# Performance work log

Measured on AMD Instinct MI355X. Metric: run time of the kernel, lower is better.

The kernel has to match this reference:

```python
import jax, jax.numpy as jnp
import numpy as np

V = 32000   # input_size == output_size (vocab)
E = 512     # embedding_dim
H = 1024    # hidden_dim
B = 32      # batch
S = 64      # source length
T = 64      # target length
SOS = 1     # Vocabulary.special_tokens['<sos>']


def setup_inputs() -> dict:
    key = jax.random.key(0)
    ks = jax.random.split(key, 24)
    sc_e = 1.0 / np.sqrt(H)
    d = {
        'input_seq': jax.random.randint(ks[0], (B, S), 0, V),
        'target_seq': jax.random.randint(ks[1], (B, T), 0, V),
        'emb': jax.random.normal(ks[2], (V, E), jnp.float32) * 0.02,
        'fc_W': jax.random.normal(ks[3], (V, H), jnp.float32) * sc_e,
        'fc_b': jnp.zeros((V,), jnp.float32),
    }
    i = 4
    for pre in ('enc', 'dec'):
        for l, in_dim in ((0, E), (1, H)):
            d[f'{pre}_Wih{l}'] = jax.random.normal(ks[i], (4 * H, in_dim), jnp.float32) * sc_e; i += 1
            d[f'{pre}_Whh{l}'] = jax.random.normal(ks[i], (4 * H, H), jnp.float32) * sc_e; i += 1
            d[f'{pre}_bih{l}'] = jnp.zeros((4 * H,), jnp.float32)
            d[f'{pre}_bhh{l}'] = jnp.zeros((4 * H,), jnp.float32)
    return d


def _lstm_cell(x, h, c, Wih, Whh, bih, bhh):
    # PyTorch gate order: i, f, g, o
    g = x @ Wih.T + h @ Whh.T + (bih + bhh)
    i, f, gg, o = jnp.split(g, 4, axis=-1)
    c = jax.nn.sigmoid(f) * c + jax.nn.sigmoid(i) * jnp.tanh(gg)
    h = jax.nn.sigmoid(o) * jnp.tanh(c)
    return h, c


def _run_lstm(x_tbe, h0, c0, h1, c1, Wih0, Whh0, bih0, bhh0, Wih1, Whh1, bih1, bhh1):
    # x_tbe: [T, B, in]; 2-layer LSTM, returns top-layer hiddens [T, B, H] and final state
    def step(carry, x_t):
        h0, c0, h1, c1 = carry
        h0, c0 = _lstm_cell(x_t, h0, c0, Wih0, Whh0, bih0, bhh0)
        h1, c1 = _lstm_cell(h0, h1, c1, Wih1, Whh1, bih1, bhh1)
        return (h0, c0, h1, c1), h1
    carry, hs = jax.lax.scan(step, (h0, c0, h1, c1), x_tbe)
    return carry, hs


def reference(input_seq, target_seq, emb, fc_W, fc_b,
              enc_Wih0, enc_Whh0, enc_bih0, enc_bhh0,
              enc_Wih1, enc_Whh1, enc_bih1, enc_bhh1,
              dec_Wih0, dec_Whh0, dec_bih0, dec_bhh0,
              dec_Wih1, dec_Whh1, dec_bih1, dec_bhh1):
    b = input_seq.shape[0]
    z = jnp.zeros((b, H), emb.dtype)
    # --- encoder over source sequence ---
    enc_in = emb[input_seq].transpose(1, 0, 2)  # [S, B, E]
    (h0, c0, h1, c1), _ = _run_lstm(enc_in, z, z, z, z,
                                    enc_Wih0, enc_Whh0, enc_bih0, enc_bhh0,
                                    enc_Wih1, enc_Whh1, enc_bih1, enc_bhh1)
    # --- decoder: full teacher forcing -> inputs are [<sos>, target[:, :-1]] ---
    dec_ids = jnp.concatenate([jnp.full((b, 1), SOS, target_seq.dtype),
                               target_seq[:, :-1]], axis=1)
    dec_in = emb[dec_ids].transpose(1, 0, 2)  # [T, B, E]
    _, dec_hs = _run_lstm(dec_in, h0, c0, h1, c1,
                          dec_Wih0, dec_Whh0, dec_bih0, dec_bhh0,
                          dec_Wih1, dec_Whh1, dec_bih1, dec_bhh1)
    # fc applied per step (linear, so one batched matmul is identical math)
    logits = jnp.einsum('tbh,vh->btv', dec_hs, fc_W) + fc_b  # [B, T, V]
    return logits
```

## Files before the change

### kernel.cpp

```cpp
#include <hip/hip_runtime.h>

#define DEVINL __device__ __forceinline__

typedef unsigned short u16;
typedef __attribute__((ext_vector_type(8))) short v8s;
typedef __attribute__((ext_vector_type(4))) short v4s;
typedef __attribute__((ext_vector_type(4))) float v4f;

static constexpr int Vn = 32000, En = 512, Hn = 1024, Bn = 32, Tn = 64;
static constexpr int FH = 4096;
static constexpr int MR = 2048;
static constexpr int BH = Bn * Hn;

DEVINL u16 f2bf(float x) {
    unsigned u = __float_as_uint(x);
    return (u16)((u + 0x7FFFu + ((u >> 16) & 1u)) >> 16);
}
DEVINL float bf2f(u16 h) { return __uint_as_float(((unsigned)h) << 16); }
DEVINL void split2(float x, u16 &hi, u16 &lo) {
    u16 h = f2bf(x);
    hi = h;
    lo = f2bf(x - bf2f(h));
}
DEVINL float sigm(float x) { return 1.f / (1.f + __expf(-x)); }
DEVINL float tanh_fast(float x) { return 1.f - 2.f / (__expf(2.f * x) + 1.f); }
DEVINL v4f mf(v8s a, v8s b, v4f c) { return __builtin_amdgcn_mfma_f32_16x16x32_bf16(a, b, c, 0, 0, 0); }
DEVINL v8s cat8(v4s a, v4s b) { return __builtin_shufflevector(a, b, 0, 1, 2, 3, 4, 5, 6, 7); }

DEVINL void gload_lds16(const u16* g, u16* l) {
    __builtin_amdgcn_global_load_lds((const __attribute__((address_space(1))) void*)g,
                                     (__attribute__((address_space(3))) void*)l, 16, 0, 0);
}

static constexpr int BAR_U32 = 16 + 256 * 16 + 256 * 16;
__global__ void bar_init(unsigned* bar) {
    for (int i = threadIdx.x; i < BAR_U32; i += 256) bar[i] = 0u;
}

__global__ void gather_split(const float* __restrict__ emb, const int* __restrict__ seq,
                             int isdec, u16* __restrict__ xh, u16* __restrict__ xl) {
    const int m = blockIdx.x;
    const int b = m & 31, t = m >> 5;
    const int id = isdec ? (t == 0 ? 1 : seq[b * 64 + t - 1]) : seq[b * 64 + t];
    const float* src = emb + (size_t)id * En;
    for (int e = threadIdx.x; e < En; e += 256) {
        u16 h, l; split2(src[e], h, l);
        xh[(size_t)m * En + e] = h;
        xl[(size_t)m * En + e] = l;
    }
}

__global__ void split_w(const float* __restrict__ W, u16* __restrict__ hi,
                        u16* __restrict__ lo, int n4) {
    const int stride = gridDim.x * blockDim.x;
    for (int i = blockIdx.x * blockDim.x + threadIdx.x; i < n4; i += stride) {
        float4 x = ((const float4*)W)[i];
        u16 h0,h1,h2,h3,l0,l1,l2,l3;
        split2(x.x,h0,l0); split2(x.y,h1,l1); split2(x.z,h2,l2); split2(x.w,h3,l3);
        ushort4 hv; hv.x=h0; hv.y=h1; hv.z=h2; hv.w=h3;
        ((ushort4*)hi)[i] = hv;
        if (lo) { ushort4 lv; lv.x=l0; lv.y=l1; lv.z=l2; lv.w=l3; ((ushort4*)lo)[i] = lv; }
    }
}

__global__ void perm_split(const float* __restrict__ Whh, u16* __restrict__ ph,
                           u16* __restrict__ pl) {
    const int g = blockIdx.x;
    const int q = g >> 10, j = g & 1023;
    const int dst = (j >> 2) * 16 + q * 4 + (j & 3);
    const int k4 = threadIdx.x;
    float4 x = ((const float4*)(Whh + (size_t)g * Hn))[k4];
    u16 h0,h1,h2,h3,l0,l1,l2,l3;
    split2(x.x,h0,l0); split2(x.y,h1,l1); split2(x.z,h2,l2); split2(x.w,h3,l3);
    ushort4 hv; hv.x=h0; hv.y=h1; hv.z=h2; hv.w=h3;
    ushort4 lv; lv.x=l0; lv.y=l1; lv.z=l2; lv.w=l3;
    ((ushort4*)(ph + (size_t)dst * Hn))[k4] = hv;
    ((ushort4*)(pl + (size_t)dst * Hn))[k4] = lv;
}

__global__ void unperm_h(const u16* __restrict__ ph, const u16* __restrict__ pl,
                         u16* __restrict__ oh, u16* __restrict__ ol) {
    const int m = blockIdx.x, t = m >> 5, b = m & 31;
    const int e = threadIdx.x;
    const size_t src = (size_t)t * BH + (size_t)e * 128 + b * 4;
    const size_t dst = (size_t)m * Hn + (size_t)e * 4;
    *(v4s*)(oh + dst) = *(const v4s*)(ph + src);
    *(v4s*)(ol + dst) = *(const v4s*)(pl + src);
}

template<int TERMS, int MODE>
__global__ __launch_bounds__(256)
void gemm_bt(const u16* __restrict__ Ahi, const u16* __restrict__ Alo,
             const u16* __restrict__ Bhi, const u16* __restrict__ Blo,
             const float* __restrict__ bias1, const float* __restrict__ bias2,
             float* __restrict__ Cout, int M, int N, int K) {
    constexpr bool AL = (TERMS >= 2), BL = (TERMS >= 3);
    __shared__ __align__(16) u16 sAh[128 * 32];
    __shared__ __align__(16) u16 sBh[128 * 32];
    __shared__ __align__(16) u16 sAl[AL ? 128 * 32 : 8];
    __shared__ __align__(16) u16 sBl[BL ? 128 * 32 : 8];

    const int tid = threadIdx.x;
    const int lane = tid & 63, wave = tid >> 6;
    const int wr = wave >> 1, wc = wave & 1;
    const int nwgx = gridDim.x;
    const int nwg = nwgx * gridDim.y;
    int wg = blockIdx.y * nwgx + blockIdx.x;
    wg = (wg & 7) * (nwg >> 3) + (wg >> 3);
    const int m0 = (wg / nwgx) * 128, n0 = (wg % nwgx) * 128;
    const int fr = lane & 15, fk = lane >> 4;

    v4f acc[4][4];
#pragma unroll
    for (int i = 0; i < 4; ++i)
#pragma unroll
        for (int j = 0; j < 4; ++j) acc[i][j] = (v4f){0.f, 0.f, 0.f, 0.f};

    const int c0 = tid, c1 = tid + 256;
    const int r0 = c0 >> 2, kg0 = c0 & 3, r1 = c1 >> 2, kg1 = c1 & 3;
    const int cw0 = (tid & ~63) * 8;
    const int cw1 = cw0 + 256 * 8;

    for (int kk = 0; kk < K; kk += 32) {
        const size_t a0 = (size_t)(m0 + r0) * K + kk + kg0 * 8;
        const size_t a1 = (size_t)(m0 + r1) * K + kk + kg1 * 8;
        const size_t b0 = (size_t)(n0 + r0) * K + kk + kg0 * 8;
        const size_t b1 = (size_t)(n0 + r1) * K + kk + kg1 * 8;
        gload_lds16(Ahi + a0, sAh + cw0);
        gload_lds16(Ahi + a1, sAh + cw1);
        gload_lds16(Bhi + b0, sBh + cw0);
        gload_lds16(Bhi + b1, sBh + cw1);
        if constexpr (AL) {
            gload_lds16(Alo + a0, sAl + cw0);
            gload_lds16(Alo + a1, sAl + cw1);
        }
        if constexpr (BL) {
            gload_lds16(Blo + b0, sBl + cw0);
            gload_lds16(Blo + b1, sBl + cw1);
        }
        __syncthreads();

        v8s ah[4], bh[4], al[4], bl[4];
#pragma unroll
        for (int mt = 0; mt < 4; ++mt) {
            const int row = wr * 64 + mt * 16 + fr;
            const int idx = row * 32 + fk * 8;
            ah[mt] = *(const v8s*)(sAh + idx);
            if constexpr (AL) al[mt] = *(const v8s*)(sAl + idx);
        }
#pragma unroll
        for (int nt = 0; nt < 4; ++nt) {
            const int row = wc * 64 + nt * 16 + fr;
            const int idx = row * 32 + fk * 8;
            bh[nt] = *(const v8s*)(sBh + idx);
            if constexpr (BL) bl[nt] = *(const v8s*)(sBl + idx);
        }
#pragma unroll
        for (int mt = 0; mt < 4; ++mt)
#pragma unroll
            for (int nt = 0; nt < 4; ++nt) {
                acc[mt][nt] = mf(ah[mt], bh[nt], acc[mt][nt]);
                if constexpr (AL) acc[mt][nt] = mf(al[mt], bh[nt], acc[mt][nt]);
                if constexpr (BL) acc[mt][nt] = mf(ah[mt], bl[nt], acc[mt][nt]);
            }
        __syncthreads();
    }

#pragma unroll
    for (int nt = 0; nt < 4; ++nt) {
        const int col = n0 + wc * 64 + nt * 16 + fr;
        float bsum = bias1 ? bias1[col] : 0.f;
        if (bias2) bsum += bias2[col];
#pragma unroll
        for (int mt = 0; mt < 4; ++mt) {
            const int rowb = m0 + wr * 64 + mt * 16 + fk * 4;
#pragma unroll
            for (int p = 0; p < 4; ++p) {
                const int row = rowb + p;
                const float v = acc[mt][nt][p] + bsum;
                if constexpr (MODE == 2) {
                    const int t = row >> 5, b = row & 31;
                    Cout[(size_t)b * ((size_t)Tn * Vn) + (size_t)t * Vn + col] = v;
                } else if constexpr (MODE == 1) {
                    const int q = col >> 10, j = col & 1023;
                    const int bidw = j >> 2, rloc = (j & 3) * 4 + q;
                    Cout[(size_t)bidw * ((size_t)MR * 16) + (size_t)row * 16 + rloc] = v;
                } else {
                    Cout[(size_t)row * N + col] = v;
                }
            }
        }
    }
}

DEVINL void wait_flags(unsigned* flags, unsigned tgt) {
    if (threadIdx.x < 256) {
        while (__hip_atomic_load(&flags[threadIdx.x * 16], __ATOMIC_RELAXED, __HIP_MEMORY_SCOPE_AGENT) < tgt)
            __builtin_amdgcn_s_sleep(1);
    }
    __syncthreads();
}
DEVINL void signal_phase(unsigned* flags, unsigned val) {
    __syncthreads();
    if (threadIdx.x == 0)
        __hip_atomic_store(&flags[blockIdx.x * 16], val, __ATOMIC_RELAXED, __HIP_MEMORY_SCOPE_AGENT);
}

#define DECLW(P) v8s P##0, P##1, P##2, P##3
#define LOADW(P, BASE) do { const u16* _b = (BASE) + woff; \
    P##0 = *(const v8s*)(_b);       P##1 = *(const v8s*)(_b + 32); \
    P##2 = *(const v8s*)(_b + 64);  P##3 = *(const v8s*)(_b + 96); } while (0)
#define PINW(P) asm volatile("" : "+v"(P##0), "+v"(P##1), "+v"(P##2), "+v"(P##3))

#define LD8(B, B0, RO) cat8(*(const v4s*)((B) + (size_t)(B0) * 128 + (RO)), \
                            *(const v4s*)((B) + (size_t)(B0) * 128 + 128 + (RO)))

#define KT0(K) { \
    const int b0 = wave * 32 + K * 8 + fk * 2; \
    v8s hah = LD8(h0sh, b0, fr4); \
    v8s hal = LD8(h0sl, b0, fr4); \
    v8s hbh = LD8(h0sh, b0, fr4 + 64); \
    v8s hbl = LD8(h0sl, b0, fr4 + 64); \
    if (doL0) { \
        r0a = mf(hah, w0h_##K, r0a); r0a = mf(hal, w0h_##K, r0a); r0a = mf(hah, w0l_##K, r0a); \
        r0b = mf(hbh, w0h_##K, r0b); r0b = mf(hbl, w0h_##K, r0b); r0b = mf(hbh, w0l_##K, r0b); } \
    if (doL1) { \
        r1a = mf(hah, wih_##K, r1a); r1a = mf(hal, wih_##K, r1a); r1a = mf(hah, wil_##K, r1a); \
        r1b = mf(hbh, wih_##K, r1b); r1b = mf(hbl, wih_##K, r1b); r1b = mf(hbh, wil_##K, r1b); } }

#define KT1(K) { \
    const int b0 = wave * 32 + K * 8 + fk * 2; \
    v8s hah = LD8(h1sh, b0, fr4); \
    v8s hal = LD8(h1sl, b0, fr4); \
    v8s hbh = LD8(h1sh, b0, fr4 + 64); \
    v8s hbl = LD8(h1sl, b0, fr4 + 64); \
    r1a = mf(hah, w1h_##K, r1a); r1a = mf(hal, w1h_##K, r1a); r1a = mf(hah, w1l_##K, r1a); \
    r1b = mf(hbh, w1h_##K, r1b); r1b = mf(hbl, w1h_##K, r1b); r1b = mf(hbh, w1l_##K, r1b); }

__global__ __launch_bounds__(512, 2)
void lstm_scan2(const u16* __restrict__ W0h, const u16* __restrict__ W0l,
                const u16* __restrict__ WIh, const u16* __restrict__ WIl,
                const u16* __restrict__ W1h, const u16* __restrict__ W1l,
                const float* __restrict__ G0,
                const float* __restrict__ bi1, const float* __restrict__ bh1,
                const u16* __restrict__ s0h, const u16* __restrict__ s0l,
                const u16* __restrict__ s1h, const u16* __restrict__ s1l,
                u16* __restrict__ h0ha, u16* __restrict__ h0la,
                u16* __restrict__ h1ha, u16* __restrict__ h1la,
                u16* __restrict__ hs_h, u16* __restrict__ hs_l,
                const float* __restrict__ c0i, const float* __restrict__ c1i,
                float* __restrict__ c0o, float* __restrict__ c1o,
                unsigned* bar, int pbase, int initfs) {
    __shared__ float red0[8][32][17];
    __shared__ float red1[8][32][17];
    const int tid = threadIdx.x, lane = tid & 63, wave = tid >> 6, bid = blockIdx.x;
    const int fr = lane & 15, fk = lane >> 4;
    const int fr4 = fr * 4;
    const size_t woff = (size_t)(bid * 16 + fr) * Hn + wave * 128 + fk * 8;
    unsigned* flagsA = bar + 16;
    unsigned* flagsB = bar + 16 + 256 * 16;

    DECLW(w0h_); DECLW(w0l_); DECLW(wih_); DECLW(wil_); DECLW(w1h_); DECLW(w1l_);
    LOADW(w0h_, W0h); LOADW(w0l_, W0l);
    LOADW(wih_, WIh); LOADW(wil_, WIl);
    LOADW(w1h_, W1h); LOADW(w1l_, W1l);
    PINW(w0h_); PINW(w0l_); PINW(wih_); PINW(wil_); PINW(w1h_); PINW(w1l_);

    const int lt = tid & 127, cb = lt >> 2, cu = lt & 3, cj = bid * 4 + cu;
    const bool isL0 = tid < 128;
    const bool isL1 = (tid >= 128) && (tid < 256);
    float creg = 0.f;
    float b1v[4];
    if (isL0) {
        if (initfs) creg = c0i[cb * Hn + cj];
    } else if (isL1) {
        if (initfs) creg = c1i[cb * Hn + cj];
#pragma unroll
        for (int q = 0; q < 4; ++q) b1v[q] = bi1[q * Hn + cj] + bh1[q * Hn + cj];
    }

    for (int p = 0; p <= 64; ++p) {
        const bool doL0 = (p < 64), doL1 = (p >= 1);
        const bool hasH0 = (p > 0) || (initfs != 0);
        const bool hasH1 = doL1 && ((p > 1) || (initfs != 0));
        const u16* h0sh = (p == 0) ? s0h : h0ha + (size_t)(p - 1) * BH;
        const u16* h0sl = (p == 0) ? s0l : h0la + (size_t)(p - 1) * BH;
        const u16* h1sh = (p <= 1) ? s1h : h1ha + (size_t)(p - 2) * BH;
        const u16* h1sl = (p <= 1) ? s1l : h1la + (size_t)(p - 2) * BH;

        v4f gq = (v4f){0.f, 0.f, 0.f, 0.f};
        if (isL0 && doL0)
            gq = *(const v4f*)(G0 + (size_t)bid * ((size_t)MR * 16)
                               + (size_t)(p * 32 + cb) * 16 + cu * 4);

        if (p >= 1) wait_flags(flagsA, (unsigned)(pbase + p));

        v4f r0a = {0,0,0,0}, r0b = {0,0,0,0}, r1a = {0,0,0,0}, r1b = {0,0,0,0};
        if (hasH0) {
            KT0(0) KT0(1) KT0(2) KT0(3)
        }
        if (doL0 && hasH0) {
#pragma unroll
            for (int pp = 0; pp < 4; ++pp) {
                red0[wave][fk * 4 + pp][fr]      = r0a[pp];
                red0[wave][fk * 4 + pp + 16][fr] = r0b[pp];
            }
        }
        __syncthreads();

        if (isL0 && doL0) {
            float gv[4];
#pragma unroll
            for (int q = 0; q < 4; ++q) {
                const int rr = q * 4 + cu;
                float s = 0.f;
                if (hasH0) {
#pragma unroll
                    for (int wv = 0; wv < 8; ++wv) s += red0[wv][cb][rr];
                }
                gv[q] = s + gq[q];
            }
            const float gi = sigm(gv[0]), gf = sigm(gv[1]);
            const float gg = tanh_fast(gv[2]), go = sigm(gv[3]);
            creg = gf * creg + gi * gg;
            const float h = go * tanh_fast(creg);
            u16 hh, hl; split2(h, hh, hl);
            const unsigned prh = (unsigned)(u16)__shfl_xor((int)hh, 1);
            const unsigned prl = (unsigned)(u16)__shfl_xor((int)hl, 1);
            if ((cu & 1) == 0) {
                const size_t ho2 = (size_t)p * (BH / 2) + bid * 64 + cb * 2 + (cu >> 1);
                __hip_atomic_store((unsigned*)h0ha + ho2, (prh << 16) | hh,
                                   __ATOMIC_RELAXED, __HIP_MEMORY_SCOPE_AGENT);
                __hip_atomic_store((unsigned*)h0la + ho2, (prl << 16) | hl,
                                   __ATOMIC_RELAXED, __HIP_MEMORY_SCOPE_AGENT);
            }
            if (p == 63) {
                c0o[cb * Hn + cj] = creg;
                if (hs_h) {
                    hs_h[bid * 128 + cb * 4 + cu] = hh;
                    hs_l[bid * 128 + cb * 4 + cu] = hl;
                }
            }
        }
        signal_phase(flagsA, (unsigned)(pbase + p + 1));

        if (p >= 2) wait_flags(flagsB, (unsigned)(pbase + p));

        if (hasH1) {
            KT1(0) KT1(1) KT1(2) KT1(3)
        }
        if (doL1) {
#pragma unroll
            for (int pp = 0; pp < 4; ++pp) {
                red1[wave][fk * 4 + pp][fr]      = r1a[pp];
                red1[wave][fk * 4 + pp + 16][fr] = r1b[pp];
            }
        }
        __syncthreads();

        if (isL1 && doL1) {
            const int t1 = p - 1;
            float gv[4];
#pragma unroll
            for (int q = 0; q < 4; ++q) {
                const int rr = q * 4 + cu;
                float s = b1v[q];
#pragma unroll
                for (int wv = 0; wv < 8; ++wv) s += red1[wv][cb][rr];
                gv[q] = s;
            }
            const float gi = sigm(gv[0]), gf = sigm(gv[1]);
            const float gg = tanh_fast(gv[2]), go = sigm(gv[3]);
            creg = gf * creg + gi * gg;
            const float h = go * tanh_fast(creg);
            u16 hh, hl; split2(h, hh, hl);
            const unsigned prh = (unsigned)(u16)__shfl_xor((int)hh, 1);
            const unsigned prl = (unsigned)(u16)__shfl_xor((int)hl, 1);
            if ((cu & 1) == 0) {
                const size_t ho2 = (size_t)t1 * (BH / 2) + bid * 64 + cb * 2 + (cu >> 1);
                __hip_atomic_store((unsigned*)h1ha + ho2, (prh << 16) | hh,
                                   __ATOMIC_RELAXED, __HIP_MEMORY_SCOPE_AGENT);
                __hip_atomic_store((unsigned*)h1la + ho2, (prl << 16) | hl,
                                   __ATOMIC_RELAXED, __HIP_MEMORY_SCOPE_AGENT);
            }
            if (t1 == 63) c1o[cb * Hn + cj] = creg;
        }
        signal_phase(flagsB, (unsigned)(pbase + p + 1));
    }
}

extern "C" void kernel_launch(void* const* d_in, const int* in_sizes, int n_in,
                              void* d_out, int out_size, void* d_ws, size_t ws_size,
                              hipStream_t stream) {
    (void)in_sizes; (void)n_in; (void)out_size; (void)ws_size;
    const int*   input_seq  = (const int*)d_in[0];
    const int*   target_seq = (const int*)d_in[1];
    const float* emb  = (const float*)d_in[2];
    const float* fc_W = (const float*)d_in[3];
    const float* fc_b = (const float*)d_in[4];
    const float* W_ih[4] = {(const float*)d_in[5],  (const float*)d_in[9],
                            (const float*)d_in[13], (const float*)d_in[17]};
    const float* W_hh[4] = {(const float*)d_in[6],  (const float*)d_in[10],
                            (const float*)d_in[14], (const float*)d_in[18]};
    const float* b_ih[4] = {(const float*)d_in[7],  (const float*)d_in[11],
                            (const float*)d_in[15], (const float*)d_in[19]};
    const float* b_hh[4] = {(const float*)d_in[8],  (const float*)d_in[12],
                            (const float*)d_in[16], (const float*)d_in[20]};

    char* w = (char*)d_ws;
    size_t off = 0;
    auto alloc = [&](size_t bytes) {
        void* p = (void*)(w + off);
        off += (bytes + 255) & ~(size_t)255;
        return p;
    };
    unsigned* bar = (unsigned*)alloc(BAR_U32 * 4);
    float* G   = (float*)alloc((size_t)MR * FH * 4);
    u16* W0h   = (u16*)alloc((size_t)FH * Hn * 2);
    u16* W0l   = (u16*)alloc((size_t)FH * Hn * 2);
    u16* WIh   = (u16*)alloc((size_t)FH * Hn * 2);
    u16* WIl   = (u16*)alloc((size_t)FH * Hn * 2);
    u16* W1h   = (u16*)alloc((size_t)FH * Hn * 2);
    u16* W1l   = (u16*)alloc((size_t)FH * Hn * 2);
    u16* SWh   = (u16*)alloc((size_t)FH * Hn * 2);
    u16* SWl   = (u16*)alloc((size_t)FH * Hn * 2);
    u16* Xh    = (u16*)alloc((size_t)MR * En * 2);
    u16* Xl    = (u16*)alloc((size_t)MR * En * 2);
    u16* hAh   = (u16*)alloc((size_t)Tn * BH * 2);
    u16* hAl   = (u16*)alloc((size_t)Tn * BH * 2);
    u16* hBh   = (u16*)alloc((size_t)Tn * BH * 2);
    u16* hBl   = (u16*)alloc((size_t)Tn * BH * 2);
    u16* hs0h  = (u16*)alloc((size_t)BH * 2);
    u16* hs0l  = (u16*)alloc((size_t)BH * 2);
    float* c0  = (float*)alloc((size_t)BH * 4);
    float* c1  = (float*)alloc((size_t)BH * 4);
    u16* hFh   = (u16*)alloc((size_t)MR * Hn * 2);
    u16* hFl   = (u16*)alloc((size_t)MR * Hn * 2);
    u16* fWh = (u16*)G;

    bar_init<<<1, 256, 0, stream>>>(bar);

    auto scan = [&](const u16* s0hp, const u16* s0lp, const u16* s1hp, const u16* s1lp,
                    u16* hsh, u16* hsl, const float* bi1, const float* bh1,
                    int pbase, int fs) {
        const u16 *a0=W0h,*a1=W0l,*a2=WIh,*a3=WIl,*a4=W1h,*a5=W1l;
        const float* Gp = G;
        u16 *p0=hAh,*p1=hAl,*p2=hBh,*p3=hBl;
        const float *ci0=c0,*ci1=c1; float *co0=c0,*co1=c1;
        unsigned* bp = bar;
        void* args[] = {(void*)&a0,(void*)&a1,(void*)&a2,(void*)&a3,(void*)&a4,(void*)&a5,
                        (void*)&Gp,(void*)&bi1,(void*)&bh1,
                        (void*)&s0hp,(void*)&s0lp,(void*)&s1hp,(void*)&s1lp,
                        (void*)&p0,(void*)&p1,(void*)&p2,(void*)&p3,
                        (void*)&hsh,(void*)&hsl,
                        (void*)&ci0,(void*)&ci1,(void*)&co0,(void*)&co1,
                        (void*)&bp,(void*)&pbase,(void*)&fs};
        if (hipLaunchCooperativeKernel((void*)lstm_scan2, dim3(256), dim3(512),
                                       args, 0, stream) != hipSuccess) {
            lstm_scan2<<<dim3(256), dim3(512), 0, stream>>>(
                W0h, W0l, WIh, WIl, W1h, W1l, G, bi1, bh1,
                s0hp, s0lp, s1hp, s1lp, hAh, hAl, hBh, hBl, hsh, hsl,
                c0, c1, c0, c1, bar, pbase, fs);
        }
    };

    const size_t lastT = (size_t)63 * BH;

    gather_split<<<MR, 256, 0, stream>>>(emb, input_seq, 0, Xh, Xl);
    split_w<<<2048, 256, 0, stream>>>(W_ih[0], SWh, SWl, FH * En / 4);
    gemm_bt<3, 1><<<dim3(FH / 128, MR / 128), 256, 0, stream>>>(
        Xh, Xl, SWh, SWl, b_ih[0], b_hh[0], G, MR, FH, En);
    perm_split<<<FH, 256, 0, stream>>>(W_hh[0], W0h, W0l);
    perm_split<<<FH, 256, 0, stream>>>(W_ih[1], WIh, WIl);
    perm_split<<<FH, 256, 0, stream>>>(W_hh[1], W1h, W1l);
    scan(hs0h, hs0l, hs0h, hs0l, hs0h, hs0l, b_ih[1], b_hh[1], 0, 0);

    gather_split<<<MR, 256, 0, stream>>>(emb, target_seq, 1, Xh, Xl);
    split_w<<<2048, 256, 0, stream>>>(W_ih[2], SWh, SWl, FH * En / 4);
    gemm_bt<3, 1><<<dim3(FH / 128, MR / 128), 256, 0, stream>>>(
        Xh, Xl, SWh, SWl, b_ih[2], b_hh[2], G, MR, FH, En);
    perm_split<<<FH, 256, 0, stream>>>(W_hh[2], W0h, W0l);
    perm_split<<<FH, 256, 0, stream>>>(W_ih[3], WIh, WIl);
    perm_split<<<FH, 256, 0, stream>>>(W_hh[3], W1h, W1l);
    scan(hs0h, hs0l, hBh + lastT, hBl + lastT, nullptr, nullptr,
         b_ih[3], b_hh[3], 130, 1);

    unperm_h<<<MR, 256, 0, stream>>>(hBh, hBl, hFh, hFl);
    split_w<<<2048, 256, 0, stream>>>(fc_W, fWh, nullptr, Vn * Hn / 4);
    gemm_bt<2, 2><<<dim3(Vn / 128, MR / 128), 256, 0, stream>>>(
        hFh, hFl, fWh, nullptr, fc_b, nullptr, (float*)d_out, MR, Vn, Hn);
}
```

Measured before the change: 1.431 ms.

## Split LSTM scan block into layer-0 and layer-1 wave groups with LDS barriers

The persistent LSTM scan kernel previously ran both layers in lockstep across all 8 waves, using block-wide __syncthreads and grid flag waits. Now waves 0-3 handle layer 0 alone, with its recurrent weights held in registers, and waves 4-7 handle layer 1. The layer-1 waves stream their input and recurrent weights from global memory each step. The two groups sync through LDS atomic counters instead of __syncthreads, so layer 0 of step t+1 can overlap layer 1 of step t. The trade is reloading layer-1 weights from memory every step, plus spin-wait overhead and more reliance on careful memory ordering.

New measurement: 2.185 ms. 1.53x slower.

```diff
diff --git a/kernel.cpp b/kernel.cpp
--- a/kernel.cpp
+++ b/kernel.cpp
@@ -193,49 +193,64 @@
     }
 }
 
-DEVINL void wait_flags(unsigned* flags, unsigned tgt) {
-    if (threadIdx.x < 256) {
-        while (__hip_atomic_load(&flags[threadIdx.x * 16], __ATOMIC_RELAXED, __HIP_MEMORY_SCOPE_AGENT) < tgt)
+DEVINL void poll4(unsigned* flags, unsigned tgt, int lane) {
+#pragma unroll
+    for (int j = 0; j < 4; ++j) {
+        unsigned* p = flags + (size_t)(lane + j * 64) * 16;
+        while (__hip_atomic_load(p, __ATOMIC_RELAXED, __HIP_MEMORY_SCOPE_AGENT) < tgt)
             __builtin_amdgcn_s_sleep(1);
     }
-    __syncthreads();
-}
-DEVINL void signal_phase(unsigned* flags, unsigned val) {
-    __syncthreads();
-    if (threadIdx.x == 0)
-        __hip_atomic_store(&flags[blockIdx.x * 16], val, __ATOMIC_RELAXED, __HIP_MEMORY_SCOPE_AGENT);
-}
-
-#define DECLW(P) v8s P##0, P##1, P##2, P##3
-#define LOADW(P, BASE) do { const u16* _b = (BASE) + woff; \
+}
+DEVINL void lds_arrive(unsigned* c) {
+    __hip_atomic_fetch_add(c, 1u, __ATOMIC_RELEASE, __HIP_MEMORY_SCOPE_WORKGROUP);
+}
+DEVINL void lds_spin(unsigned* c, unsigned tgt) {
+    while (__hip_atomic_load(c, __ATOMIC_ACQUIRE, __HIP_MEMORY_SCOPE_WORKGROUP) < tgt)
+        __builtin_amdgcn_s_sleep(0);
+}
+
+#define DECLW8(P) v8s P##0, P##1, P##2, P##3, P##4, P##5, P##6, P##7
+#define LOADW8(P, BASE) do { const u16* _b = (BASE) + woff; \
     P##0 = *(const v8s*)(_b);       P##1 = *(const v8s*)(_b + 32); \
-    P##2 = *(const v8s*)(_b + 64);  P##3 = *(const v8s*)(_b + 96); } while (0)
-#define PINW(P) asm volatile("" : "+v"(P##0), "+v"(P##1), "+v"(P##2), "+v"(P##3))
+    P##2 = *(const v8s*)(_b + 64);  P##3 = *(const v8s*)(_b + 96); \
+    P##4 = *(const v8s*)(_b + 128); P##5 = *(const v8s*)(_b + 160); \
+    P##6 = *(const v8s*)(_b + 192); P##7 = *(const v8s*)(_b + 224); } while (0)
+#define PINW8(P) asm volatile("" : "+v"(P##0), "+v"(P##1), "+v"(P##2), "+v"(P##3), \
+                                   "+v"(P##4), "+v"(P##5), "+v"(P##6), "+v"(P##7))
 
 #define LD8(B, B0, RO) cat8(*(const v4s*)((B) + (size_t)(B0) * 128 + (RO)), \
                             *(const v4s*)((B) + (size_t)(B0) * 128 + 128 + (RO)))
 
-#define KT0(K) { \
-    const int b0 = wave * 32 + K * 8 + fk * 2; \
+#define KT0L(K) { \
+    const int b0 = wave * 64 + K * 8 + fk * 2; \
     v8s hah = LD8(h0sh, b0, fr4); \
     v8s hal = LD8(h0sl, b0, fr4); \
     v8s hbh = LD8(h0sh, b0, fr4 + 64); \
     v8s hbl = LD8(h0sl, b0, fr4 + 64); \
-    if (doL0) { \
-        r0a = mf(hah, w0h_##K, r0a); r0a = mf(hal, w0h_##K, r0a); r0a = mf(hah, w0l_##K, r0a); \
-        r0b = mf(hbh, w0h_##K, r0b); r0b = mf(hbl, w0h_##K, r0b); r0b = mf(hbh, w0l_##K, r0b); } \
-    if (doL1) { \
-        r1a = mf(hah, wih_##K, r1a); r1a = mf(hal, wih_##K, r1a); r1a = mf(hah, wil_##K, r1a); \
-        r1b = mf(hbh, wih_##K, r1b); r1b = mf(hbl, wih_##K, r1b); r1b = mf(hbh, wil_##K, r1b); } }
-
-#define KT1(K) { \
-    const int b0 = wave * 32 + K * 8 + fk * 2; \
+    r0a = mf(hah, w0h_##K, r0a); r0a = mf(hal, w0h_##K, r0a); r0a = mf(hah, w0l_##K, r0a); \
+    r0b = mf(hbh, w0h_##K, r0b); r0b = mf(hbl, w0h_##K, r0b); r0b = mf(hbh, w0l_##K, r0b); }
+
+#define KTIH(K) { \
+    const int b0 = w4 * 64 + K * 8 + fk * 2; \
+    v8s wih = *(const v8s*)(WIh + woffT + K * 32); \
+    v8s wil = *(const v8s*)(WIl + woffT + K * 32); \
+    v8s hah = LD8(h0sh, b0, fr4); \
+    v8s hal = LD8(h0sl, b0, fr4); \
+    v8s hbh = LD8(h0sh, b0, fr4 + 64); \
+    v8s hbl = LD8(h0sl, b0, fr4 + 64); \
+    r1a = mf(hah, wih, r1a); r1a = mf(hal, wih, r1a); r1a = mf(hah, wil, r1a); \
+    r1b = mf(hbh, wih, r1b); r1b = mf(hbl, wih, r1b); r1b = mf(hbh, wil, r1b); }
+
+#define KTH1(K) { \
+    const int b0 = w4 * 64 + K * 8 + fk * 2; \
+    v8s w1h = *(const v8s*)(W1h + woffT + K * 32); \
+    v8s w1l = *(const v8s*)(W1l + woffT + K * 32); \
     v8s hah = LD8(h1sh, b0, fr4); \
     v8s hal = LD8(h1sl, b0, fr4); \
     v8s hbh = LD8(h1sh, b0, fr4 + 64); \
     v8s hbl = LD8(h1sl, b0, fr4 + 64); \
-    r1a = mf(hah, w1h_##K, r1a); r1a = mf(hal, w1h_##K, r1a); r1a = mf(hah, w1l_##K, r1a); \
-    r1b = mf(hbh, w1h_##K, r1b); r1b = mf(hbl, w1h_##K, r1b); r1b = mf(hbh, w1l_##K, r1b); }
+    r1a = mf(hah, w1h, r1a); r1a = mf(hal, w1h, r1a); r1a = mf(hah, w1l, r1a); \
+    r1b = mf(hbh, w1h, r1b); r1b = mf(hbl, w1h, r1b); r1b = mf(hbh, w1l, r1b); }
 
 __global__ __launch_bounds__(512, 2)
 void lstm_scan2(const u16* __restrict__ W0h, const u16* __restrict__ W0l,
@@ -251,141 +266,151 @@
                 const float* __restrict__ c0i, const float* __restrict__ c1i,
                 float* __restrict__ c0o, float* __restrict__ c1o,
                 unsigned* bar, int pbase, int initfs) {
-    __shared__ float red0[8][32][17];
-    __shared__ float red1[8][32][17];
+    __shared__ float red0[4][32][17];
+    __shared__ float red1[4][32][17];
+    __shared__ unsigned cb4[4];
     const int tid = threadIdx.x, lane = tid & 63, wave = tid >> 6, bid = blockIdx.x;
     const int fr = lane & 15, fk = lane >> 4;
     const int fr4 = fr * 4;
-    const size_t woff = (size_t)(bid * 16 + fr) * Hn + wave * 128 + fk * 8;
     unsigned* flagsA = bar + 16;
     unsigned* flagsB = bar + 16 + 256 * 16;
-
-    DECLW(w0h_); DECLW(w0l_); DECLW(wih_); DECLW(wil_); DECLW(w1h_); DECLW(w1l_);
-    LOADW(w0h_, W0h); LOADW(w0l_, W0l);
-    LOADW(wih_, WIh); LOADW(wil_, WIl);
-    LOADW(w1h_, W1h); LOADW(w1l_, W1l);
-    PINW(w0h_); PINW(w0l_); PINW(wih_); PINW(wil_); PINW(w1h_); PINW(w1l_);
-
-    const int lt = tid & 127, cb = lt >> 2, cu = lt & 3, cj = bid * 4 + cu;
-    const bool isL0 = tid < 128;
-    const bool isL1 = (tid >= 128) && (tid < 256);
-    float creg = 0.f;
-    float b1v[4];
-    if (isL0) {
-        if (initfs) creg = c0i[cb * Hn + cj];
-    } else if (isL1) {
-        if (initfs) creg = c1i[cb * Hn + cj];
-#pragma unroll
-        for (int q = 0; q < 4; ++q) b1v[q] = bi1[q * Hn + cj] + bh1[q * Hn + cj];
-    }
-
-    for (int p = 0; p <= 64; ++p) {
-        const bool doL0 = (p < 64), doL1 = (p >= 1);
-        const bool hasH0 = (p > 0) || (initfs != 0);
-        const bool hasH1 = doL1 && ((p > 1) || (initfs != 0));
-        const u16* h0sh = (p == 0) ? s0h : h0ha + (size_t)(p - 1) * BH;
-        const u16* h0sl = (p == 0) ? s0l : h0la + (size_t)(p - 1) * BH;
-        const u16* h1sh = (p <= 1) ? s1h : h1ha + (size_t)(p - 2) * BH;
-        const u16* h1sl = (p <= 1) ? s1l : h1la + (size_t)(p - 2) * BH;
-
-        v4f gq = (v4f){0.f, 0.f, 0.f, 0.f};
-        if (isL0 && doL0)
-            gq = *(const v4f*)(G0 + (size_t)bid * ((size_t)MR * 16)
-                               + (size_t)(p * 32 + cb) * 16 + cu * 4);
-
-        if (p >= 1) wait_flags(flagsA, (unsigned)(pbase + p));
-
-        v4f r0a = {0,0,0,0}, r0b = {0,0,0,0}, r1a = {0,0,0,0}, r1b = {0,0,0,0};
-        if (hasH0) {
-            KT0(0) KT0(1) KT0(2) KT0(3)
-        }
-        if (doL0 && hasH0) {
+    if (tid == 0) { cb4[0] = 0; cb4[1] = 0; cb4[2] = 0; cb4[3] = 0; }
+    __syncthreads();
+
+    if (wave < 4) {
+        const size_t woff = (size_t)(bid * 16 + fr) * Hn + wave * 256 + fk * 8;
+        DECLW8(w0h_); DECLW8(w0l_);
+        LOADW8(w0h_, W0h); LOADW8(w0l_, W0l);
+        PINW8(w0h_); PINW8(w0l_);
+        const int lt = tid & 127, cbb = lt >> 2, cu = lt & 3, cj = bid * 4 + cu;
+        const bool isCell = tid < 128;
+        float creg = 0.f;
+        if (isCell && initfs) creg = c0i[cbb * Hn + cj];
+
+        for (int q = 0; q < 64; ++q) {
+            v4f gq = (v4f){0.f, 0.f, 0.f, 0.f};
+            if (isCell)
+                gq = *(const v4f*)(G0 + (size_t)bid * ((size_t)MR * 16)
+                                   + (size_t)(q * 32 + cbb) * 16 + cu * 4);
+            if (q >= 1) poll4(flagsA, (unsigned)(pbase + q), lane);
+            const bool hasH0 = (q > 0) || (initfs != 0);
+            const u16* h0sh = (q == 0) ? s0h : h0ha + (size_t)(q - 1) * BH;
+            const u16* h0sl = (q == 0) ? s0l : h0la + (size_t)(q - 1) * BH;
+            v4f r0a = {0,0,0,0}, r0b = {0,0,0,0};
+            if (hasH0) {
+                KT0L(0) KT0L(1) KT0L(2) KT0L(3) KT0L(4) KT0L(5) KT0L(6) KT0L(7)
+            }
 #pragma unroll
             for (int pp = 0; pp < 4; ++pp) {
                 red0[wave][fk * 4 + pp][fr]      = r0a[pp];
                 red0[wave][fk * 4 + pp + 16][fr] = r0b[pp];
             }
-        }
-        __syncthreads();
-
-        if (isL0 && doL0) {
-            float gv[4];
-#pragma unroll
-            for (int q = 0; q < 4; ++q) {
-                const int rr = q * 4 + cu;
-                float s = 0.f;
-                if (hasH0) {
-#pragma unroll
-                    for (int wv = 0; wv < 8; ++wv) s += red0[wv][cb][rr];
-                }
-                gv[q] = s + gq[q];
-            }
-            const float gi = sigm(gv[0]), gf = sigm(gv[1]);
-            const float gg = tanh_fast(gv[2]), go = sigm(gv[3]);
-            creg = gf * creg + gi * gg;
-            const float h = go * tanh_fast(creg);
-            u16 hh, hl; split2(h, hh, hl);
-            const unsigned prh = (unsigned)(u16)__shfl_xor((int)hh, 1);
-            const unsigned prl = (unsigned)(u16)__shfl_xor((int)hl, 1);
-            if ((cu & 1) == 0) {
-                const size_t ho2 = (size_t)p * (BH / 2) + bid * 64 + cb * 2 + (cu >> 1);
-                __hip_atomic_store((unsigned*)h0ha + ho2, (prh << 16) | hh,
-                                   __ATOMIC_RELAXED, __HIP_MEMORY_SCOPE_AGENT);
-                __hip_atomic_store((unsigned*)h0la + ho2, (prl << 16) | hl,
-                                   __ATOMIC_RELAXED, __HIP_MEMORY_SCOPE_AGENT);
-            }
-            if (p == 63) {
-                c0o[cb * Hn + cj] = creg;
-                if (hs_h) {
-                    hs_h[bid * 128 + cb * 4 + cu] = hh;
-                    hs_l[bid * 128 + cb * 4 + cu] = hl;
-                }
-            }
-        }
-        signal_phase(flagsA, (unsigned)(pbase + p + 1));
-
-        if (p >= 2) wait_flags(flagsB, (unsigned)(pbase + p));
-
-        if (hasH1) {
-            KT1(0) KT1(1) KT1(2) KT1(3)
-        }
-        if (doL1) {
+            if (lane == 0) lds_arrive(&cb4[0]);
+            if (isCell) {
+                lds_spin(&cb4[0], 4u * (q + 1));
+                float gv[4];
+#pragma unroll
+                for (int qg = 0; qg < 4; ++qg) {
+                    const int rr = qg * 4 + cu;
+                    gv[qg] = red0[0][cbb][rr] + red0[1][cbb][rr]
+                           + red0[2][cbb][rr] + red0[3][cbb][rr] + gq[qg];
+                }
+                const float gi = sigm(gv[0]), gf = sigm(gv[1]);
+                const float gg = tanh_fast(gv[2]), go = sigm(gv[3]);
+                creg = gf * creg + gi * gg;
+                const float h = go * tanh_fast(creg);
+                u16 hh, hl; split2(h, hh, hl);
+                const unsigned prh = (unsigned)(u16)__shfl_xor((int)hh, 1);
+                const unsigned prl = (unsigned)(u16)__shfl_xor((int)hl, 1);
+                if ((cu & 1) == 0) {
+                    const size_t ho2 = (size_t)q * (BH / 2) + bid * 64 + cbb * 2 + (cu >> 1);
+                    __hip_atomic_store((unsigned*)h0ha + ho2, (prh << 16) | hh,
+                                       __ATOMIC_RELAXED, __HIP_MEMORY_SCOPE_AGENT);
+                    __hip_atomic_store((unsigned*)h0la + ho2, (prl << 16) | hl,
+                                       __ATOMIC_RELAXED, __HIP_MEMORY_SCOPE_AGENT);
+                }
+                if (q == 63) {
+                    c0o[cbb * Hn + cj] = creg;
+                    if (hs_h) {
+                        hs_h[bid * 128 + cbb * 4 + cu] = hh;
+                        hs_l[bid * 128 + cbb * 4 + cu] = hl;
+                    }
+                }
+                asm volatile("s_waitcnt vmcnt(0)" ::: "memory");
+                if (lane == 0) lds_arrive(&cb4[1]);
+                if (tid == 0) {
+                    lds_spin(&cb4[1], 2u * (q + 1));
+                    __hip_atomic_store(&flagsA[bid * 16], (unsigned)(pbase + q + 1),
+                                       __ATOMIC_RELAXED, __HIP_MEMORY_SCOPE_AGENT);
+                }
+            }
+        }
+    } else {
+        const int w4 = wave - 4;
+        const size_t woffT = (size_t)(bid * 16 + fr) * Hn + w4 * 256 + fk * 8;
+        const int lt = (tid - 256) & 127, cbb = lt >> 2, cu = lt & 3, cj = bid * 4 + cu;
+        const bool isCell1 = (tid >= 256) && (tid < 384);
+        float creg = 0.f;
+        float b1v[4] = {0.f, 0.f, 0.f, 0.f};
+        if (isCell1) {
+            if (initfs) creg = c1i[cbb * Hn + cj];
+#pragma unroll
+            for (int qg = 0; qg < 4; ++qg) b1v[qg] = bi1[qg * Hn + cj] + bh1[qg * Hn + cj];
+        }
+
+        for (int q = 1; q <= 64; ++q) {
+            const int t1 = q - 1;
+            poll4(flagsA, (unsigned)(pbase + q), lane);
+            if (q >= 2) poll4(flagsB, (unsigned)(pbase + q), lane);
+            const bool hasH1 = (q > 1) || (initfs != 0);
+            const u16* h0sh = h0ha + (size_t)(q - 1) * BH;
+            const u16* h0sl = h0la + (size_t)(q - 1) * BH;
+            const u16* h1sh = (q <= 1) ? s1h : h1ha + (size_t)(q - 2) * BH;
+            const u16* h1sl = (q <= 1) ? s1l : h1la + (size_t)(q - 2) * BH;
+            v4f r1a = {0,0,0,0}, r1b = {0,0,0,0};
+            KTIH(0) KTIH(1) KTIH(2) KTIH(3) KTIH(4) KTIH(5) KTIH(6) KTIH(7)
+            if (hasH1) {
+                KTH1(0) KTH1(1) KTH1(2) KTH1(3) KTH1(4) KTH1(5) KTH1(6) KTH1(7)
+            }
 #pragma unroll
             for (int pp = 0; pp < 4; ++pp) {
-                red1[wave][fk * 4 + pp][fr]      = r1a[pp];
-                red1[wave][fk * 4 + pp + 16][fr] = r1b[pp];
-            }
-        }
-        __syncthreads();
-
-        if (isL1 && doL1) {
-            const int t1 = p - 1;
-            float gv[4];
-#pragma unroll
-            for (int q = 0; q < 4; ++q) {
-                const int rr = q * 4 + cu;
-                float s = b1v[q];
-#pragma unroll
-                for (int wv = 0; wv < 8; ++wv) s += red1[wv][cb][rr];
-                gv[q] = s;
-            }
-            const float gi = sigm(gv[0]), gf = sigm(gv[1]);
-            const float gg = tanh_fast(gv[2]), go = sigm(gv[3]);
-            creg = gf * creg + gi * gg;
-            const float h = go * tanh_fast(creg);
-            u16 hh, hl; split2(h, hh, hl);
-            const unsigned prh = (unsigned)(u16)__shfl_xor((int)hh, 1);
-            const unsigned prl = (unsigned)(u16)__shfl_xor((int)hl, 1);
-            if ((cu & 1) == 0) {
-                const size_t ho2 = (size_t)t1 * (BH / 2) + bid * 64 + cb * 2 + (cu >> 1);
-                __hip_atomic_store((unsigned*)h1ha + ho2, (prh << 16) | hh,
-                                   __ATOMIC_RELAXED, __HIP_MEMORY_SCOPE_AGENT);
-                __hip_atomic_store((unsigned*)h1la + ho2, (prl << 16) | hl,
-                                   __ATOMIC_RELAXED, __HIP_MEMORY_SCOPE_AGENT);
-            }
-            if (t1 == 63) c1o[cb * Hn + cj] = creg;
-        }
-        signal_phase(flagsB, (unsigned)(pbase + p + 1));
+                red1[w4][fk * 4 + pp][fr]      = r1a[pp];
+                red1[w4][fk * 4 + pp + 16][fr] = r1b[pp];
+            }
+            if (lane == 0) lds_arrive(&cb4[2]);
+            if (isCell1) {
+                lds_spin(&cb4[2], 4u * q);
+                float gv[4];
+#pragma unroll
+                for (int qg = 0; qg < 4; ++qg) {
+                    const int rr = qg * 4 + cu;
+                    gv[qg] = red1[0][cbb][rr] + red1[1][cbb][rr]
+                           + red1[2][cbb][rr] + red1[3][cbb][rr] + b1v[qg];
+                }
+                const float gi = sigm(gv[0]), gf = sigm(gv[1]);
+                const float gg = tanh_fast(gv[2]), go = sigm(gv[3]);
+                creg = gf * creg + gi * gg;
+                const float h = go * tanh_fast(creg);
+                u16 hh, hl; split2(h, hh, hl);
+                const unsigned prh = (unsigned)(u16)__shfl_xor((int)hh, 1);
+                const unsigned prl = (unsigned)(u16)__shfl_xor((int)hl, 1);
+                if ((cu & 1) == 0) {
+                    const size_t ho2 = (size_t)t1 * (BH / 2) + bid * 64 + cbb * 2 + (cu >> 1);
+                    __hip_atomic_store((unsigned*)h1ha + ho2, (prh << 16) | hh,
+                                       __ATOMIC_RELAXED, __HIP_MEMORY_SCOPE_AGENT);
+                    __hip_atomic_store((unsigned*)h1la + ho2, (prl << 16) | hl,
+                                       __ATOMIC_RELAXED, __HIP_MEMORY_SCOPE_AGENT);
+                }
+                if (t1 == 63) c1o[cbb * Hn + cj] = creg;
+                asm volatile("s_waitcnt vmcnt(0)" ::: "memory");
+                if (lane == 0) lds_arrive(&cb4[3]);
+                if (tid == 256) {
+                    lds_spin(&cb4[3], 2u * q);
+                    __hip_atomic_store(&flagsB[bid * 16], (unsigned)(pbase + q + 1),
+                                       __ATOMIC_RELAXED, __HIP_MEMORY_SCOPE_AGENT);
+                }
+            }
+        }
     }
 }
 
@@ -483,7 +508,7 @@
     perm_split<<<FH, 256, 0, stream>>>(W_ih[3], WIh, WIl);
     perm_split<<<FH, 256, 0, stream>>>(W_hh[3], W1h, W1l);
     scan(hs0h, hs0l, hBh + lastT, hBl + lastT, nullptr, nullptr,
-         b_ih[3], b_hh[3], 130, 1);
+         b_ih[3], b_hh[3], 70, 1);
 
     unperm_h<<<MR, 256, 0, stream>>>(hBh, hBl, hFh, hFl);
     split_w<<<2048, 256, 0, stream>>>(fc_W, fWh, nullptr, Vn * Hn / 4);
```
